# Optimization experiments

Measured on AMD Instinct MI355X. Metric: run time of the kernel, lower is better.

The kernel has to match this reference:

```python
import jax, jax.numpy as jnp
import numpy as np

NUM_CLASSES = 36   # len(linspace(0, 35, 36))
K = 50             # num_class_sample
TEMP = 0.1
BASE_TEMP = 0.07


def setup_inputs() -> dict:
    key = jax.random.key(0)
    k1, k2 = jax.random.split(key)
    B, D, H, W = 8, 32, 256, 256
    embedding = jax.random.normal(k1, (B, D, H, W), dtype=jnp.float32)
    label_map = jax.random.randint(k2, (B, H, W), 0, NUM_CLASSES, dtype=jnp.int32)
    return {"embedding": embedding, "label_map": label_map}


def reference(embedding, label_map):
    B, D, H, W = embedding.shape
    N = H * W
    feats = embedding.reshape(B, D, N).transpose(0, 2, 1)            # [B,N,D]
    labels = label_map.reshape(B, N)
    cls = jnp.arange(NUM_CLASSES)

    # ---- per-class mean prototypes (seg queue), vectorized scatter-mean ----
    onehot = (labels[:, :, None] == cls[None, None, :]).astype(feats.dtype)  # [B,N,C]
    counts = onehot.sum(1)                                           # [B,C]
    seg = jnp.einsum('bnc,bnd->bcd', onehot, feats) / jnp.maximum(counts, 1.0)[:, :, None]
    seg_valid = counts > 0                                           # [B,C]

    # ---- first-K-occurrences pixel sample per class (deterministic perm) ----
    pos = jnp.arange(N, dtype=jnp.int32)
    # matching pixels sort to the front, per class
    keys = jnp.where(labels[:, None, :] == cls[None, :, None],
                     pos[None, None, :], N + pos[None, None, :])      # [B,C,N]
    order = jnp.argsort(keys, axis=-1)[..., :K]                       # [B,C,K]
    pix = feats[jnp.arange(B)[:, None, None], order]                  # [B,C,K,D]
    pix_valid = jnp.arange(K)[None, None, :] < counts[:, :, None]     # [B,C,K]

    P = NUM_CLASSES * K
    pix_x = pix.reshape(B, P, D)
    pix_v = pix_valid.reshape(B, P).astype(feats.dtype)
    pix_label = jnp.repeat(cls, K)                                    # [P]

    # ---- masked InfoNCE-style contrastive loss ----
    logits = jnp.einsum('bpd,bcd->bpc', pix_x, seg) / TEMP            # [B,P,C]
    col_valid = seg_valid[:, None, :]                                 # [B,1,C]
    col_valid_f = col_valid.astype(feats.dtype)
    masked = jnp.where(col_valid, logits, -jnp.inf)
    logits = logits - jax.lax.stop_gradient(masked.max(-1, keepdims=True))
    pos_mask = ((pix_label[None, :, None] == cls[None, None, :]).astype(feats.dtype)
                * col_valid_f)                                        # [B,P,C]
    exp_l = jnp.exp(logits) * col_valid_f
    neg = (exp_l * (1.0 - pos_mask)).sum(-1, keepdims=True)
    log_prob = logits - jnp.log(exp_l + neg)
    mean_lpp = (pos_mask * log_prob).sum(-1) / jnp.maximum(pos_mask.sum(-1), 1.0)
    loss_p = -(TEMP / BASE_TEMP) * mean_lpp                           # [B,P]
    per_batch = (loss_p * pix_v).sum(-1) / jnp.maximum(pix_v.sum(-1), 1.0)
    return per_batch.mean()  # loss_weight = 1
```

## Files before the change

### kernel.cpp

```cpp
#include <hip/hip_runtime.h>

#define NCLS 36
#define KSEL 50
#define BATCH 8
#define DIM 32
#define NPIX 65536
#define TEMP_ 0.1f
#define BASE_TEMP_ 0.07f
#define ROWS (NCLS*KSEL)
#define BLOCKS_PER_B 29

__global__ __launch_bounds__(256) void kA(const float* __restrict__ emb,
                                          const int* __restrict__ lab,
                                          float* __restrict__ seg_sum,
                                          int* __restrict__ counts,
                                          int* __restrict__ order,
                                          float* __restrict__ loss_num)
{
    __shared__ float smem[256 * 37];
    const int bid = blockIdx.x;
    const int tid = threadIdx.x;

    if (bid < 256) {
        const int b = bid >> 5, d = bid & 31;
        const float4* __restrict__ src  = (const float4*)(emb + (size_t)(b * DIM + d) * NPIX);
        const int4*   __restrict__ lsrc = (const int4*)(lab + (size_t)b * NPIX);
        float* acc = smem + tid * 37;
        #pragma unroll
        for (int c = 0; c < 37; ++c) acc[c] = 0.f;
        for (int i = 0; i < NPIX / 1024; ++i) {
            const int idx = i * 256 + tid;
            float4 v = src[idx];
            int4   l = lsrc[idx];
            acc[l.x] += v.x; acc[l.y] += v.y; acc[l.z] += v.z; acc[l.w] += v.w;
        }
        __syncthreads();
        if (tid < NCLS) {
            float s = 0.f;
            for (int t = 0; t < 256; ++t) s += smem[t * 37 + tid];
            seg_sum[((size_t)b * NCLS + tid) * DIM + d] = s;
        }
    } else if (bid < 264) {
        const int b = bid - 256;
        int* acc = (int*)smem + tid * 37;
        #pragma unroll
        for (int c = 0; c < 37; ++c) acc[c] = 0;
        const int4* __restrict__ lsrc = (const int4*)(lab + (size_t)b * NPIX);
        for (int i = 0; i < NPIX / 1024; ++i) {
            int4 l = lsrc[i * 256 + tid];
            acc[l.x]++; acc[l.y]++; acc[l.z]++; acc[l.w]++;
        }
        __syncthreads();
        if (tid < NCLS) {
            int s = 0;
            for (int t = 0; t < 256; ++t) s += ((int*)smem)[t * 37 + tid];
            counts[b * NCLS + tid] = s;
        }
        if (b == 0 && tid < BATCH) loss_num[tid] = 0.f;
    } else {
        const int idx = bid - 264;
        const int b = idx / NCLS, c = idx % NCLS;
        if (tid < 64) {
            const int* __restrict__ lb = lab + (size_t)b * NPIX;
            int* __restrict__ dst = order + ((size_t)b * NCLS + c) * KSEL;
            int found = 0;
            for (int n0 = 0; n0 < NPIX && found < KSEL; n0 += 64) {
                const int n = n0 + tid;
                const int match = (lb[n] == c);
                const unsigned long long m = __ballot(match);
                if (match) {
                    const int r = found + __popcll(m & ((1ull << tid) - 1ull));
                    if (r < KSEL) dst[r] = n;
                }
                found += __popcll(m);
            }
        }
    }
}

__global__ __launch_bounds__(64) void kB(const float* __restrict__ emb,
                                         const int* __restrict__ counts_g,
                                         const int* __restrict__ order_g,
                                         const float* __restrict__ seg_sum,
                                         float* __restrict__ loss_num)
{
    __shared__ float seg[NCLS * DIM];
    __shared__ int   cnt[NCLS];
    const int b = blockIdx.x / BLOCKS_PER_B;
    const int chunk = blockIdx.x % BLOCKS_PER_B;
    const int tid = threadIdx.x;

    if (tid < NCLS) cnt[tid] = counts_g[b * NCLS + tid];
    __syncthreads();
    for (int i = tid; i < NCLS * DIM; i += 64) {
        const float cn = (float)max(cnt[i >> 5], 1);
        seg[i] = seg_sum[(size_t)b * NCLS * DIM + i] / cn;
    }
    __syncthreads();

    const int p = chunk * 64 + tid;
    float loss = 0.f;
    if (p < ROWS) {
        const int crow = p / KSEL;
        const int k = p - crow * KSEL;
        if (k < cnt[crow]) {
            const int n = order_g[((size_t)b * NCLS + crow) * KSEL + k];
            float f[DIM];
            const float* __restrict__ eb = emb + (size_t)b * DIM * NPIX + n;
            #pragma unroll
            for (int d = 0; d < DIM; ++d) f[d] = eb[(size_t)d * NPIX];

            float m = -1e30f, s = 0.f, lrow = 0.f;
            for (int c = 0; c < NCLS; ++c) {
                if (cnt[c] > 0) {
                    float acc = 0.f;
                    const float4* sp = (const float4*)(seg + c * DIM);
                    #pragma unroll
                    for (int q = 0; q < 8; ++q) {
                        float4 sv = sp[q];
                        acc += f[q*4+0]*sv.x + f[q*4+1]*sv.y
                             + f[q*4+2]*sv.z + f[q*4+3]*sv.w;
                    }
                    const float l = acc * (1.0f / TEMP_);
                    if (c == crow) lrow = l;
                    const float nm = fmaxf(m, l);
                    s = s * expf(m - nm) + expf(l - nm);
                    m = nm;
                }
            }
            loss = -(TEMP_ / BASE_TEMP_) * (lrow - m - logf(s));
        }
    }
    #pragma unroll
    for (int o = 32; o > 0; o >>= 1) loss += __shfl_down(loss, o);
    if (tid == 0) atomicAdd(&loss_num[b], loss);
}

__global__ void kC(const float* __restrict__ loss_num,
                   const int* __restrict__ counts,
                   float* __restrict__ out)
{
    if (blockIdx.x == 0 && threadIdx.x == 0) {
        float total = 0.f;
        for (int b = 0; b < BATCH; ++b) {
            int den = 0;
            for (int c = 0; c < NCLS; ++c) den += min(counts[b * NCLS + c], KSEL);
            total += loss_num[b] / (float)max(den, 1);
        }
        out[0] = total / (float)BATCH;
    }
}

extern "C" void kernel_launch(void* const* d_in, const int* in_sizes, int n_in,
                              void* d_out, int out_size, void* d_ws, size_t ws_size,
                              hipStream_t stream)
{
    const float* emb = (const float*)d_in[0];
    const int*   lab = (const int*)d_in[1];

    float* seg_sum  = (float*)d_ws;
    int*   counts   = (int*)(seg_sum + BATCH * NCLS * DIM);
    int*   order    = counts + BATCH * NCLS;
    float* loss_num = (float*)(order + BATCH * NCLS * KSEL);
    float* out      = (float*)d_out;

    kA<<<552, 256, 0, stream>>>(emb, lab, seg_sum, counts, order, loss_num);
    kB<<<BATCH * BLOCKS_PER_B, 64, 0, stream>>>(emb, counts, order, seg_sum, loss_num);
    kC<<<1, 1, 0, stream>>>(loss_num, counts, out);
}
```

Baseline: 126.8 us.

## Use LDS atomics for histograms, parallelize reductions, prefetch labels, widen kB blocks

In kA, the per-thread LDS histogram updates become atomicAdd on LDS, and the final 256-way column sum is split across 144 threads in four partial groups. The first-K sampling loop now prefetches the next label before the current ballot. kB moves from 64-thread to 256-thread blocks with 8 chunks per batch, and kC becomes a wave-level shuffle reduction. The LDS atomics add cost on private (non-shared) slots, while the other changes target reduction serialization and launch shape.

```diff
diff --git a/kernel.cpp b/kernel.cpp
--- a/kernel.cpp
+++ b/kernel.cpp
@@ -8,7 +8,7 @@
 #define TEMP_ 0.1f
 #define BASE_TEMP_ 0.07f
 #define ROWS (NCLS*KSEL)
-#define BLOCKS_PER_B 29
+#define CHUNKS_PER_B 8
 
 __global__ __launch_bounds__(256) void kA(const float* __restrict__ emb,
                                           const int* __restrict__ lab,
@@ -17,7 +17,8 @@
                                           int* __restrict__ order,
                                           float* __restrict__ loss_num)
 {
-    __shared__ float smem[256 * 37];
+    __shared__ float smem[256 * 37 + 4 * 36];
+    float* __restrict__ red = smem + 256 * 37;
     const int bid = blockIdx.x;
     const int tid = threadIdx.x;
 
@@ -32,29 +33,49 @@
             const int idx = i * 256 + tid;
             float4 v = src[idx];
             int4   l = lsrc[idx];
-            acc[l.x] += v.x; acc[l.y] += v.y; acc[l.z] += v.z; acc[l.w] += v.w;
+            atomicAdd(&acc[l.x], v.x);
+            atomicAdd(&acc[l.y], v.y);
+            atomicAdd(&acc[l.z], v.z);
+            atomicAdd(&acc[l.w], v.w);
+        }
+        __syncthreads();
+        if (tid < 144) {
+            const int c = tid % NCLS, q = tid / NCLS;
+            float s = 0.f;
+            #pragma unroll
+            for (int t = 0; t < 64; ++t) s += smem[(q * 64 + t) * 37 + c];
+            red[q * NCLS + c] = s;
         }
         __syncthreads();
         if (tid < NCLS) {
-            float s = 0.f;
-            for (int t = 0; t < 256; ++t) s += smem[t * 37 + tid];
+            const float s = red[tid] + red[NCLS + tid] + red[2 * NCLS + tid] + red[3 * NCLS + tid];
             seg_sum[((size_t)b * NCLS + tid) * DIM + d] = s;
         }
     } else if (bid < 264) {
         const int b = bid - 256;
-        int* acc = (int*)smem + tid * 37;
+        int* iacc = (int*)smem + tid * 37;
         #pragma unroll
-        for (int c = 0; c < 37; ++c) acc[c] = 0;
+        for (int c = 0; c < 37; ++c) iacc[c] = 0;
         const int4* __restrict__ lsrc = (const int4*)(lab + (size_t)b * NPIX);
         for (int i = 0; i < NPIX / 1024; ++i) {
             int4 l = lsrc[i * 256 + tid];
-            acc[l.x]++; acc[l.y]++; acc[l.z]++; acc[l.w]++;
+            atomicAdd(&iacc[l.x], 1);
+            atomicAdd(&iacc[l.y], 1);
+            atomicAdd(&iacc[l.z], 1);
+            atomicAdd(&iacc[l.w], 1);
+        }
+        __syncthreads();
+        if (tid < 144) {
+            const int c = tid % NCLS, q = tid / NCLS;
+            int s = 0;
+            #pragma unroll
+            for (int t = 0; t < 64; ++t) s += ((int*)smem)[(q * 64 + t) * 37 + c];
+            ((int*)red)[q * NCLS + c] = s;
         }
         __syncthreads();
         if (tid < NCLS) {
-            int s = 0;
-            for (int t = 0; t < 256; ++t) s += ((int*)smem)[t * 37 + tid];
-            counts[b * NCLS + tid] = s;
+            const int* ired = (const int*)red;
+            counts[b * NCLS + tid] = ired[tid] + ired[NCLS + tid] + ired[2 * NCLS + tid] + ired[3 * NCLS + tid];
         }
         if (b == 0 && tid < BATCH) loss_num[tid] = 0.f;
     } else {
@@ -64,13 +85,15 @@
             const int* __restrict__ lb = lab + (size_t)b * NPIX;
             int* __restrict__ dst = order + ((size_t)b * NCLS + c) * KSEL;
             int found = 0;
+            int nxt = lb[tid];
             for (int n0 = 0; n0 < NPIX && found < KSEL; n0 += 64) {
-                const int n = n0 + tid;
-                const int match = (lb[n] == c);
+                const int cur = nxt;
+                if (n0 + 64 < NPIX) nxt = lb[n0 + 64 + tid];
+                const int match = (cur == c);
                 const unsigned long long m = __ballot(match);
                 if (match) {
                     const int r = found + __popcll(m & ((1ull << tid) - 1ull));
-                    if (r < KSEL) dst[r] = n;
+                    if (r < KSEL) dst[r] = n0 + tid;
                 }
                 found += __popcll(m);
             }
@@ -78,27 +101,27 @@
     }
 }
 
-__global__ __launch_bounds__(64) void kB(const float* __restrict__ emb,
-                                         const int* __restrict__ counts_g,
-                                         const int* __restrict__ order_g,
-                                         const float* __restrict__ seg_sum,
-                                         float* __restrict__ loss_num)
+__global__ __launch_bounds__(256) void kB(const float* __restrict__ emb,
+                                          const int* __restrict__ counts_g,
+                                          const int* __restrict__ order_g,
+                                          const float* __restrict__ seg_sum,
+                                          float* __restrict__ loss_num)
 {
     __shared__ float seg[NCLS * DIM];
     __shared__ int   cnt[NCLS];
-    const int b = blockIdx.x / BLOCKS_PER_B;
-    const int chunk = blockIdx.x % BLOCKS_PER_B;
+    const int b = blockIdx.x / CHUNKS_PER_B;
+    const int chunk = blockIdx.x % CHUNKS_PER_B;
     const int tid = threadIdx.x;
 
     if (tid < NCLS) cnt[tid] = counts_g[b * NCLS + tid];
     __syncthreads();
-    for (int i = tid; i < NCLS * DIM; i += 64) {
+    for (int i = tid; i < NCLS * DIM; i += 256) {
         const float cn = (float)max(cnt[i >> 5], 1);
         seg[i] = seg_sum[(size_t)b * NCLS * DIM + i] / cn;
     }
     __syncthreads();
 
-    const int p = chunk * 64 + tid;
+    const int p = chunk * 256 + tid;
     float loss = 0.f;
     if (p < ROWS) {
         const int crow = p / KSEL;
@@ -133,22 +156,31 @@
     }
     #pragma unroll
     for (int o = 32; o > 0; o >>= 1) loss += __shfl_down(loss, o);
-    if (tid == 0) atomicAdd(&loss_num[b], loss);
-}
-
-__global__ void kC(const float* __restrict__ loss_num,
-                   const int* __restrict__ counts,
-                   float* __restrict__ out)
-{
-    if (blockIdx.x == 0 && threadIdx.x == 0) {
-        float total = 0.f;
-        for (int b = 0; b < BATCH; ++b) {
-            int den = 0;
-            for (int c = 0; c < NCLS; ++c) den += min(counts[b * NCLS + c], KSEL);
-            total += loss_num[b] / (float)max(den, 1);
-        }
-        out[0] = total / (float)BATCH;
-    }
+    if ((tid & 63) == 0) atomicAdd(&loss_num[b], loss);
+}
+
+__global__ __launch_bounds__(64) void kC(const float* __restrict__ loss_num,
+                                         const int* __restrict__ counts,
+                                         float* __restrict__ out)
+{
+    const int lane = threadIdx.x;
+    int v[BATCH];
+    #pragma unroll
+    for (int b = 0; b < BATCH; ++b)
+        v[b] = (lane < NCLS) ? min(counts[b * NCLS + lane], KSEL) : 0;
+    const float num = (lane < BATCH) ? loss_num[lane] : 0.f;
+
+    float total = 0.f;
+    #pragma unroll
+    for (int b = 0; b < BATCH; ++b) {
+        int d = v[b];
+        #pragma unroll
+        for (int o = 32; o > 0; o >>= 1) d += __shfl_down(d, o);
+        d = __shfl(d, 0);
+        const float nb = __shfl(num, b);
+        if (lane == 0) total += nb / (float)max(d, 1);
+    }
+    if (lane == 0) out[0] = total * (1.0f / BATCH);
 }
 
 extern "C" void kernel_launch(void* const* d_in, const int* in_sizes, int n_in,
@@ -165,6 +197,6 @@
     float* out      = (float*)d_out;
 
     kA<<<552, 256, 0, stream>>>(emb, lab, seg_sum, counts, order, loss_num);
-    kB<<<BATCH * BLOCKS_PER_B, 64, 0, stream>>>(emb, counts, order, seg_sum, loss_num);
-    kC<<<1, 1, 0, stream>>>(loss_num, counts, out);
-}
+    kB<<<BATCH * CHUNKS_PER_B, 256, 0, stream>>>(emb, counts, order, seg_sum, loss_num);
+    kC<<<1, 64, 0, stream>>>(loss_num, counts, out);
+}
```

Measured after the change: 201.5 us. +58.9%, slower.
